# Optimization experiments

Hardware: AMD Instinct MI355X
Metric: run time of the kernel (lower is better)

The kernel has to match this reference:

```python
import jax, jax.numpy as jnp
import numpy as np

N_AGENTS, OBS_DIM, HID, ACT_DIM = 8192, 64, 128, 16


def setup_inputs() -> dict:
    key = jax.random.key(0)
    k = jax.random.split(key, 8)
    obs_agents = jax.random.normal(k[0], (N_AGENTS, OBS_DIM), dtype=jnp.float32)
    # binary adjacency, {0,1}, int32 (index/mask semantics, non-differentiable)
    adj = jax.random.randint(k[1], (N_AGENTS, N_AGENTS), 0, 2, dtype=jnp.int32)
    def lin(kk, fan_in, fan_out):
        lim = 1.0 / np.sqrt(fan_in)
        kw, kb = jax.random.split(kk)
        W = jax.random.uniform(kw, (fan_in, fan_out), jnp.float32, -lim, lim)
        b = jax.random.uniform(kb, (fan_out,), jnp.float32, -lim, lim)
        return W, b
    W1, b1 = lin(k[2], OBS_DIM, HID)          # encoder
    W2, b2 = lin(k[3], 2 * HID, HID)          # actor layer 1
    W3, b3 = lin(k[4], HID, ACT_DIM)          # actor layer 2
    return {"obs_agents": obs_agents, "adj": adj,
            "W1": W1, "b1": b1, "W2": W2, "b2": b2, "W3": W3, "b3": b3}


def reference(obs_agents, adj, W1, b1, W2, b2, W3, b3):
    # per-agent encode: h = tanh(obs @ W1 + b1)  -> [N, HID]
    h = jnp.tanh(obs_agents @ W1 + b1)
    # neighbor mean message: mean of h[j] over j with adj[i,j]!=0, zeros if no neighbors
    a = adj.astype(h.dtype)                      # [N, N] binary
    deg = jnp.sum(a, axis=1, keepdims=True)      # [N, 1]
    msg = (a @ h) / jnp.maximum(deg, 1.0)        # zero rows stay zero
    # actor MLP on concat([h, msg])
    combined = jnp.concatenate([h, msg], axis=-1)            # [N, 2*HID]
    hid = jnp.tanh(combined @ W2 + b2)                        # [N, HID]
    logits = hid @ W3 + b3                                    # [N, ACT_DIM]
    return logits
```

## Files before the change

kernel.cpp:

```cpp
#include <hip/hip_runtime.h>
#include <stdint.h>
#include <math.h>

#define NAG 8192
#define NC  128
#define NSPLIT 8
#define LDB2 136

typedef __attribute__((ext_vector_type(8))) short short8;
typedef __attribute__((ext_vector_type(4))) float floatx4;

__device__ __forceinline__ float bf2f(unsigned short u) {
    union { uint32_t i; float f; } v; v.i = ((uint32_t)u) << 16; return v.f;
}
__device__ __forceinline__ unsigned short f2bf(float f) {
    union { float f; uint32_t i; } v; v.f = f;
    uint32_t x = v.i;
    return (unsigned short)((x + 0x7FFFu + ((x >> 16) & 1u)) >> 16);
}
__device__ __forceinline__ unsigned short f2h(float f) {
    union { _Float16 h; unsigned short u; } v; v.h = (_Float16)f; return v.u;
}
__device__ __forceinline__ float h2f(unsigned short u) {
    union { _Float16 h; unsigned short u; } v; v.u = u; return (float)v.h;
}
__device__ __forceinline__ bool detect_f32(const void* W1, int t) {
    const unsigned short* w = (const unsigned short*)W1;
    int l = t & 63, big = 0;
    #pragma unroll
    for (int j = 0; j < 8; ++j) {
        float v = bf2f(w[l * 8 + j]);
        if (!(fabsf(v) <= 1e6f)) big = 1;
    }
    return __ballot(big) != 0ull;
}

__global__ __launch_bounds__(256) void kA_pack_encode(
    const int* __restrict__ adj,
    unsigned long long* __restrict__ bits,
    const void* __restrict__ obs,
    const void* __restrict__ W1,
    const void* __restrict__ b1,
    float* __restrict__ h_f32,
    unsigned short* __restrict__ hT)
{
    const int t = threadIdx.x;
    if (blockIdx.x < 2048) {
        const int lane = t & 63;
        const int gw = blockIdx.x * 4 + (t >> 6);
        for (int it = 0; it < 32; ++it) {
            size_t u = ((size_t)it * 8192 + gw) * 4;
            size_t col = u * 64 + lane;
            unsigned long long m0 = __ballot(adj[col]       != 0);
            unsigned long long m1 = __ballot(adj[col + 64]  != 0);
            unsigned long long m2 = __ballot(adj[col + 128] != 0);
            unsigned long long m3 = __ballot(adj[col + 192] != 0);
            if (lane == 0) {
                bits[u]     = m0;
                bits[u + 1] = m1;
                bits[u + 2] = m2;
                bits[u + 3] = m3;
            }
        }
        return;
    }
    __shared__ float obs_lds[32][68];
    __shared__ unsigned short ht_lds[128][33];
    const int abase = (blockIdx.x - 2048) * 32;
    const bool isf = detect_f32(W1, t);

    {
        int a = t >> 3, c0 = (t & 7) * 8;
        if (isf) {
            const float* p = (const float*)obs;
            #pragma unroll
            for (int j = 0; j < 8; ++j)
                obs_lds[a][c0 + j] = p[(size_t)(abase + a) * 64 + c0 + j];
        } else {
            const unsigned short* p = (const unsigned short*)obs;
            #pragma unroll
            for (int j = 0; j < 8; ++j)
                obs_lds[a][c0 + j] = bf2f(p[(size_t)(abase + a) * 64 + c0 + j]);
        }
    }
    __syncthreads();

    const int o = t & 127;
    const int half = t >> 7;
    float acc[16];
    if (isf) {
        const float* Wp = (const float*)W1;
        float bias = ((const float*)b1)[o];
        #pragma unroll
        for (int i = 0; i < 16; ++i) acc[i] = bias;
        for (int k0 = 0; k0 < 64; k0 += 8) {
            float w[8];
            #pragma unroll
            for (int j = 0; j < 8; ++j) w[j] = Wp[(k0 + j) * 128 + o];
            #pragma unroll
            for (int j = 0; j < 8; ++j)
                #pragma unroll
                for (int i = 0; i < 16; ++i)
                    acc[i] = fmaf(obs_lds[half * 16 + i][k0 + j], w[j], acc[i]);
        }
    } else {
        const unsigned short* Wp = (const unsigned short*)W1;
        float bias = bf2f(((const unsigned short*)b1)[o]);
        #pragma unroll
        for (int i = 0; i < 16; ++i) acc[i] = bias;
        for (int k0 = 0; k0 < 64; k0 += 8) {
            float w[8];
            #pragma unroll
            for (int j = 0; j < 8; ++j) w[j] = bf2f(Wp[(k0 + j) * 128 + o]);
            #pragma unroll
            for (int j = 0; j < 8; ++j)
                #pragma unroll
                for (int i = 0; i < 16; ++i)
                    acc[i] = fmaf(obs_lds[half * 16 + i][k0 + j], w[j], acc[i]);
        }
    }
    #pragma unroll
    for (int i = 0; i < 16; ++i) {
        float th = tanhf(acc[i]);
        int a = half * 16 + i;
        h_f32[(size_t)(abase + a) * 128 + o] = th;
        ht_lds[o][a] = f2bf(th);
    }
    __syncthreads();

    for (int p = 0; p < 16; ++p) {
        int n = p * 8 + (t >> 5);
        int a = t & 31;
        hT[(size_t)n * NAG + abase + a] = ht_lds[n][a];
    }
}

__global__ __launch_bounds__(256, 2) void k2_msggemm(
    const uint32_t* __restrict__ bits,
    const unsigned short* __restrict__ hT,
    unsigned short* __restrict__ Cp16)
{
    __shared__ __align__(16) unsigned short Blds[128 * LDB2];
    const int t = threadIdx.x;
    const int mtile = blockIdx.x & 63;
    const int ks = blockIdx.x >> 6;
    const int row0 = mtile * 128;
    const int kbeg = ks * 1024;

    const int wave = t >> 6, lane = t & 63;
    const int fm = lane & 15, quad = lane >> 4;

    floatx4 acc0[8], acc1[8];
    #pragma unroll
    for (int i = 0; i < 8; ++i) { acc0[i] = (floatx4)0.f; acc1[i] = (floatx4)0.f; }

    const int arow0 = row0 + wave * 32 + fm;
    const uint32_t* aWp0 = bits + (size_t)arow0 * 256 + (kbeg >> 5);
    const uint32_t* aWp1 = aWp0 + 16 * 256;

    for (int ss = 0; ss < 8; ++ss) {
        if (ss) __syncthreads();
        #pragma unroll
        for (int i = 0; i < 8; ++i) {
            int idx = i * 256 + t;
            int row = idx >> 4, ch = idx & 15;
            uint4 v = *reinterpret_cast<const uint4*>(hT + (size_t)row * NAG + kbeg + ss * 128 + ch * 8);
            *reinterpret_cast<uint4*>(&Blds[row * LDB2 + ch * 8]) = v;
        }
        int4 a0 = *reinterpret_cast<const int4*>(aWp0 + ss * 4);
        int4 a1 = *reinterpret_cast<const int4*>(aWp1 + ss * 4);
        uint32_t aw0[4] = {(uint32_t)a0.x, (uint32_t)a0.y, (uint32_t)a0.z, (uint32_t)a0.w};
        uint32_t aw1[4] = {(uint32_t)a1.x, (uint32_t)a1.y, (uint32_t)a1.z, (uint32_t)a1.w};
        __syncthreads();
        #pragma unroll
        for (int kw = 0; kw < 4; ++kw) {
            uint32_t b0 = (aw0[kw] >> (quad * 8)) & 0xFFu;
            uint32_t b1 = (aw1[kw] >> (quad * 8)) & 0xFFu;
            union { uint32_t u[4]; short8 s; } af0, af1;
            #pragma unroll
            for (int p = 0; p < 4; ++p) {
                uint32_t bb0 = b0 >> (2 * p);
                uint32_t bb1 = b1 >> (2 * p);
                af0.u[p] = ((bb0 & 1u) | ((bb0 & 2u) << 15)) * 0x3F80u;
                af1.u[p] = ((bb1 & 1u) | ((bb1 & 2u) << 15)) * 0x3F80u;
            }
            #pragma unroll
            for (int j = 0; j < 8; ++j) {
                short8 bf = *reinterpret_cast<const short8*>(&Blds[(j * 16 + fm) * LDB2 + kw * 32 + quad * 8]);
                acc0[j] = __builtin_amdgcn_mfma_f32_16x16x32_bf16(af0.s, bf, acc0[j], 0, 0, 0);
                acc1[j] = __builtin_amdgcn_mfma_f32_16x16x32_bf16(af1.s, bf, acc1[j], 0, 0, 0);
            }
        }
    }

    unsigned short* out = Cp16 + (size_t)ks * (NAG * NC);
    #pragma unroll
    for (int j = 0; j < 8; ++j) {
        int col = j * 16 + fm;
        #pragma unroll
        for (int r = 0; r < 4; ++r) {
            int row = row0 + wave * 32 + quad * 4 + r;
            out[(size_t)row * NC + col]        = f2h(acc0[j][r]);
            out[(size_t)(row + 16) * NC + col] = f2h(acc1[j][r]);
        }
    }
}

__global__ __launch_bounds__(256) void k3_actor(
    const float* __restrict__ h_f32,
    const unsigned short* __restrict__ Cp16,
    const unsigned long long* __restrict__ bits,
    const void* __restrict__ W1,
    const void* __restrict__ W2,
    const void* __restrict__ b2,
    const void* __restrict__ W3,
    const void* __restrict__ b3,
    void* __restrict__ out)
{
    __shared__ float4 comb4[8][66];
    __shared__ float hid[8][132];
    __shared__ int degp[8][33];
    __shared__ float inv_lds[8];
    const int t = threadIdx.x;
    const int abase = blockIdx.x * 8;
    const bool isf = detect_f32(W1, t);
    const size_t PS = (size_t)NAG * NC;

    {
        int a = t >> 5, j = t & 31;
        const unsigned long long* bp = bits + (size_t)(abase + a) * 128 + j * 4;
        degp[a][j] = __popcll(bp[0]) + __popcll(bp[1]) + __popcll(bp[2]) + __popcll(bp[3]);
    }
    __syncthreads();
    if (t < 8) {
        int d = 0;
        #pragma unroll
        for (int j = 0; j < 32; ++j) d += degp[t][j];
        inv_lds[t] = 1.0f / fmaxf((float)d, 1.0f);
    }
    __syncthreads();

    #pragma unroll
    for (int jj = 0; jj < 2; ++jj) {
        int idx = jj * 256 + t;
        int a = idx >> 6, q = idx & 63;
        float4 v;
        if (q < 32) {
            v = *reinterpret_cast<const float4*>(h_f32 + (size_t)(abase + a) * 128 + q * 4);
        } else {
            int f = (q - 32) * 4;
            float s0 = 0.f, s1 = 0.f, s2 = 0.f, s3 = 0.f;
            #pragma unroll
            for (int s = 0; s < NSPLIT; ++s) {
                ushort4 p = *reinterpret_cast<const ushort4*>(Cp16 + s * PS + (size_t)(abase + a) * NC + f);
                s0 += h2f(p.x); s1 += h2f(p.y); s2 += h2f(p.z); s3 += h2f(p.w);
            }
            float sc = inv_lds[a];
            v = make_float4(s0 * sc, s1 * sc, s2 * sc, s3 * sc);
        }
        comb4[a][q] = v;
    }
    __syncthreads();

    const int o = t & 127, half = t >> 7;
    float acc[4];
    if (isf) {
        const float* Wp = (const float*)W2;
        float bias = ((const float*)b2)[o];
        #pragma unroll
        for (int i = 0; i < 4; ++i) acc[i] = bias;
        for (int cq = 0; cq < 64; ++cq) {
            float w0 = Wp[(cq * 4 + 0) * 128 + o];
            float w1 = Wp[(cq * 4 + 1) * 128 + o];
            float w2 = Wp[(cq * 4 + 2) * 128 + o];
            float w3 = Wp[(cq * 4 + 3) * 128 + o];
            #pragma unroll
            for (int i = 0; i < 4; ++i) {
                float4 v = comb4[half * 4 + i][cq];
                acc[i] = fmaf(v.x, w0, acc[i]);
                acc[i] = fmaf(v.y, w1, acc[i]);
                acc[i] = fmaf(v.z, w2, acc[i]);
                acc[i] = fmaf(v.w, w3, acc[i]);
            }
        }
    } else {
        const unsigned short* Wp = (const unsigned short*)W2;
        float bias = bf2f(((const unsigned short*)b2)[o]);
        #pragma unroll
        for (int i = 0; i < 4; ++i) acc[i] = bias;
        for (int cq = 0; cq < 64; ++cq) {
            float w0 = bf2f(Wp[(cq * 4 + 0) * 128 + o]);
            float w1 = bf2f(Wp[(cq * 4 + 1) * 128 + o]);
            float w2 = bf2f(Wp[(cq * 4 + 2) * 128 + o]);
            float w3 = bf2f(Wp[(cq * 4 + 3) * 128 + o]);
            #pragma unroll
            for (int i = 0; i < 4; ++i) {
                float4 v = comb4[half * 4 + i][cq];
                acc[i] = fmaf(v.x, w0, acc[i]);
                acc[i] = fmaf(v.y, w1, acc[i]);
                acc[i] = fmaf(v.z, w2, acc[i]);
                acc[i] = fmaf(v.w, w3, acc[i]);
            }
        }
    }
    #pragma unroll
    for (int i = 0; i < 4; ++i)
        hid[half * 4 + i][o] = tanhf(acc[i]);
    __syncthreads();

    if (t < 128) {
        const int q = t & 15, ar = t >> 4;
        float l;
        if (isf) {
            const float* Wp = (const float*)W3;
            l = ((const float*)b3)[q];
            #pragma unroll 4
            for (int oo = 0; oo < 128; ++oo)
                l = fmaf(hid[ar][oo], Wp[oo * 16 + q], l);
        } else {
            const unsigned short* Wp = (const unsigned short*)W3;
            l = bf2f(((const unsigned short*)b3)[q]);
            #pragma unroll 4
            for (int oo = 0; oo < 128; ++oo)
                l = fmaf(hid[ar][oo], bf2f(Wp[oo * 16 + q]), l);
        }
        size_t i0 = (size_t)(abase + ar) * 16 + q;
        if (isf) ((float*)out)[i0] = l;
        else     ((unsigned short*)out)[i0] = f2bf(l);
    }
}

extern "C" void kernel_launch(void* const* d_in, const int* in_sizes, int n_in,
                              void* d_out, int out_size, void* d_ws, size_t ws_size,
                              hipStream_t stream) {
    const void* obs = d_in[0];
    const int*  adj = (const int*)d_in[1];
    const void* W1  = d_in[2];
    const void* b1  = d_in[3];
    const void* W2  = d_in[4];
    const void* b2  = d_in[5];
    const void* W3  = d_in[6];
    const void* b3  = d_in[7];

    char* ws = (char*)d_ws;
    unsigned short* hT   = (unsigned short*)(ws);
    float*          h_f32= (float*)(ws + 2097152);
    unsigned short* Cp16 = (unsigned short*)(ws + 6291456);
    unsigned long long* bits = (unsigned long long*)(ws + 23068672);

    hipLaunchKernelGGL(kA_pack_encode, dim3(2304), dim3(256), 0, stream,
                       adj, bits, obs, W1, b1, h_f32, hT);
    hipLaunchKernelGGL(k2_msggemm, dim3(512), dim3(256), 0, stream,
                       (const uint32_t*)bits, hT, Cp16);
    hipLaunchKernelGGL(k3_actor, dim3(1024), dim3(256), 0, stream,
                       h_f32, Cp16, bits, W1, W2, b2, W3, b3, d_out);
}
```

Measured before the change: 441.8 us.

## Split message GEMM over N halves and double-buffer LDS tile loads

The message GEMM now splits the 128 output columns into two 64-column halves per block, doubling the grid to 1024 blocks and halving accumulators so more blocks can be resident (launch bounds raised to 4). The B tile in shared memory is double-buffered: the next k-slice is loaded into registers during the MFMA loop and written to the alternate buffer, so global loads overlap compute and one barrier per step is removed. The cost is that each block re-reads the same adjacency bits and re-expands them for both column halves, which doubles that work.

```diff
diff --git a/kernel.cpp b/kernel.cpp
--- a/kernel.cpp
+++ b/kernel.cpp
@@ -135,43 +135,60 @@
     }
 }
 
-__global__ __launch_bounds__(256, 2) void k2_msggemm(
+__global__ __launch_bounds__(256, 4) void k2_msggemm(
     const uint32_t* __restrict__ bits,
     const unsigned short* __restrict__ hT,
     unsigned short* __restrict__ Cp16)
 {
-    __shared__ __align__(16) unsigned short Blds[128 * LDB2];
+    __shared__ __align__(16) unsigned short Blds[2][64 * LDB2];
     const int t = threadIdx.x;
     const int mtile = blockIdx.x & 63;
-    const int ks = blockIdx.x >> 6;
+    const int ns = (blockIdx.x >> 6) & 1;
+    const int ks = blockIdx.x >> 7;
     const int row0 = mtile * 128;
+    const int n0 = ns * 64;
     const int kbeg = ks * 1024;
 
     const int wave = t >> 6, lane = t & 63;
     const int fm = lane & 15, quad = lane >> 4;
 
-    floatx4 acc0[8], acc1[8];
-    #pragma unroll
-    for (int i = 0; i < 8; ++i) { acc0[i] = (floatx4)0.f; acc1[i] = (floatx4)0.f; }
+    floatx4 acc0[4], acc1[4];
+    #pragma unroll
+    for (int i = 0; i < 4; ++i) { acc0[i] = (floatx4)0.f; acc1[i] = (floatx4)0.f; }
 
     const int arow0 = row0 + wave * 32 + fm;
     const uint32_t* aWp0 = bits + (size_t)arow0 * 256 + (kbeg >> 5);
     const uint32_t* aWp1 = aWp0 + 16 * 256;
 
-    for (int ss = 0; ss < 8; ++ss) {
-        if (ss) __syncthreads();
-        #pragma unroll
-        for (int i = 0; i < 8; ++i) {
+    const unsigned short* hbase = hT + (size_t)n0 * NAG + kbeg;
+
+    {
+        #pragma unroll
+        for (int i = 0; i < 4; ++i) {
             int idx = i * 256 + t;
             int row = idx >> 4, ch = idx & 15;
-            uint4 v = *reinterpret_cast<const uint4*>(hT + (size_t)row * NAG + kbeg + ss * 128 + ch * 8);
-            *reinterpret_cast<uint4*>(&Blds[row * LDB2 + ch * 8]) = v;
+            uint4 v = *reinterpret_cast<const uint4*>(hbase + (size_t)row * NAG + ch * 8);
+            *reinterpret_cast<uint4*>(&Blds[0][row * LDB2 + ch * 8]) = v;
+        }
+        __syncthreads();
+    }
+
+    #pragma unroll 1
+    for (int ss = 0; ss < 8; ++ss) {
+        const int cur = ss & 1;
+        uint4 sv[4];
+        if (ss < 7) {
+            #pragma unroll
+            for (int i = 0; i < 4; ++i) {
+                int idx = i * 256 + t;
+                int row = idx >> 4, ch = idx & 15;
+                sv[i] = *reinterpret_cast<const uint4*>(hbase + (size_t)row * NAG + (ss + 1) * 128 + ch * 8);
+            }
         }
         int4 a0 = *reinterpret_cast<const int4*>(aWp0 + ss * 4);
         int4 a1 = *reinterpret_cast<const int4*>(aWp1 + ss * 4);
         uint32_t aw0[4] = {(uint32_t)a0.x, (uint32_t)a0.y, (uint32_t)a0.z, (uint32_t)a0.w};
         uint32_t aw1[4] = {(uint32_t)a1.x, (uint32_t)a1.y, (uint32_t)a1.z, (uint32_t)a1.w};
-        __syncthreads();
         #pragma unroll
         for (int kw = 0; kw < 4; ++kw) {
             uint32_t b0 = (aw0[kw] >> (quad * 8)) & 0xFFu;
@@ -185,18 +202,27 @@
                 af1.u[p] = ((bb1 & 1u) | ((bb1 & 2u) << 15)) * 0x3F80u;
             }
             #pragma unroll
-            for (int j = 0; j < 8; ++j) {
-                short8 bf = *reinterpret_cast<const short8*>(&Blds[(j * 16 + fm) * LDB2 + kw * 32 + quad * 8]);
+            for (int j = 0; j < 4; ++j) {
+                short8 bf = *reinterpret_cast<const short8*>(&Blds[cur][(j * 16 + fm) * LDB2 + kw * 32 + quad * 8]);
                 acc0[j] = __builtin_amdgcn_mfma_f32_16x16x32_bf16(af0.s, bf, acc0[j], 0, 0, 0);
                 acc1[j] = __builtin_amdgcn_mfma_f32_16x16x32_bf16(af1.s, bf, acc1[j], 0, 0, 0);
             }
         }
+        if (ss < 7) {
+            #pragma unroll
+            for (int i = 0; i < 4; ++i) {
+                int idx = i * 256 + t;
+                int row = idx >> 4, ch = idx & 15;
+                *reinterpret_cast<uint4*>(&Blds[cur ^ 1][row * LDB2 + ch * 8]) = sv[i];
+            }
+        }
+        __syncthreads();
     }
 
     unsigned short* out = Cp16 + (size_t)ks * (NAG * NC);
     #pragma unroll
-    for (int j = 0; j < 8; ++j) {
-        int col = j * 16 + fm;
+    for (int j = 0; j < 4; ++j) {
+        int col = n0 + j * 16 + fm;
         #pragma unroll
         for (int r = 0; r < 4; ++r) {
             int row = row0 + wave * 32 + quad * 4 + r;
@@ -350,7 +376,7 @@
 
     hipLaunchKernelGGL(kA_pack_encode, dim3(2304), dim3(256), 0, stream,
                        adj, bits, obs, W1, b1, h_f32, hT);
-    hipLaunchKernelGGL(k2_msggemm, dim3(512), dim3(256), 0, stream,
+    hipLaunchKernelGGL(k2_msggemm, dim3(1024), dim3(256), 0, stream,
                        (const uint32_t*)bits, hT, Cp16);
     hipLaunchKernelGGL(k3_actor, dim3(1024), dim3(256), 0, stream,
                        h_f32, Cp16, bits, W1, W2, b2, W3, b3, d_out);
```

Result: no change. 449.8 us (+1.8%).
